# Performance work log

Measured on AMD Instinct MI355X. Metric: run time of the kernel, lower is better.

## Reference

```python
import jax, jax.numpy as jnp
import numpy as np

N = 100000      # n_nodes
E = 1600000     # n_edges (avg degree 16)
IN_C = 256
OUT_C = 64
HID = OUT_C * 2  # 128


def setup_inputs() -> dict:
    key = jax.random.key(0)
    k = jax.random.split(key, 4)
    x = jax.random.normal(k[0], (N, IN_C), dtype=jnp.float32)
    edge_index = jax.random.randint(k[1], (2, E), 0, N, dtype=jnp.int64)
    W1 = jax.random.normal(k[2], (IN_C, HID), dtype=jnp.float32) * (1.0 / np.sqrt(IN_C))
    b1 = jnp.zeros((HID,), dtype=jnp.float32)
    W2 = jax.random.normal(k[3], (HID, OUT_C), dtype=jnp.float32) * (1.0 / np.sqrt(HID))
    b2 = jnp.zeros((OUT_C,), dtype=jnp.float32)
    return {"x": x, "edge_index": edge_index, "W1": W1, "b1": b1, "W2": W2, "b2": b2}


def reference(x, edge_index, W1, b1, W2, b2):
    n = x.shape[0]
    # GCNConv default: add self-loops, symmetric normalization D^-1/2 A D^-1/2
    loop = jnp.arange(n, dtype=edge_index.dtype)
    src = jnp.concatenate([edge_index[0], loop])  # [E+N]
    dst = jnp.concatenate([edge_index[1], loop])  # [E+N]
    deg = jax.ops.segment_sum(jnp.ones_like(dst, dtype=x.dtype), dst, num_segments=n)
    dis = jax.lax.rsqrt(deg)  # deg >= 1 thanks to self-loops
    norm = dis[src] * dis[dst]  # [E+N]

    def gcn_conv(h, W, b):
        h = h @ W                                   # [n, d_out] dense transform first
        msg = h[src] * norm[:, None]                # [E+N, d_out] gather + scale
        return jax.ops.segment_sum(msg, dst, num_segments=n) + b

    h = jax.nn.relu(gcn_conv(x, W1, b1))
    return gcn_conv(h, W2, b2)
```

## Files before the change

kernel.cpp:

```cpp
#include <hip/hip_runtime.h>
#include <hip/hip_bf16.h>


#define GCN_IN_C 256
#define GCN_HID  128
#define GCN_OUT  64

#define BKT_SHIFT 8
#define BKT_NODES 256
#define EPB 4096

typedef __bf16 bf16x8 __attribute__((ext_vector_type(8)));
typedef __bf16 bf16x4 __attribute__((ext_vector_type(4)));
typedef float f32x4 __attribute__((ext_vector_type(4)));

__global__ __launch_bounds__(256) void k_bucket_hist(const int* __restrict__ dst,
                                                     int* __restrict__ bcnt, int e, int nb) {
  __shared__ int h[512];
  int tid = threadIdx.x;
  h[tid] = 0; h[tid + 256] = 0;
  __syncthreads();
  int base = blockIdx.x * EPB;
#pragma unroll
  for (int j = 0; j < EPB / 256; ++j) {
    int i = base + j * 256 + tid;
    if (i < e) atomicAdd(&h[dst[i] >> BKT_SHIFT], 1);
  }
  __syncthreads();
  if (tid < nb && h[tid]) atomicAdd(&bcnt[tid], h[tid]);
  if (tid + 256 < nb && h[tid + 256]) atomicAdd(&bcnt[tid + 256], h[tid + 256]);
}

__global__ __launch_bounds__(512) void k_scan_buckets(const int* __restrict__ bcnt,
                                                      int* __restrict__ bbase,
                                                      int* __restrict__ bcur, int nb) {
  __shared__ int sh[512];
  int t = threadIdx.x;
  int v = (t < nb) ? bcnt[t] : 0;
  sh[t] = v;
  __syncthreads();
  for (int d = 1; d < 512; d <<= 1) {
    int x = (t >= d) ? sh[t - d] : 0;
    __syncthreads();
    sh[t] += x;
    __syncthreads();
  }
  if (t < nb) {
    int ex = sh[t] - v;
    bbase[t] = ex;
    bcur[t] = ex;
  }
}

__global__ __launch_bounds__(256) void k_partition(const int* __restrict__ src,
                                                   const int* __restrict__ dst,
                                                   int* __restrict__ bcur,
                                                   unsigned int* __restrict__ part,
                                                   int e, int nb) {
  __shared__ int h[512];
  __shared__ int base[512];
  int tid = threadIdx.x;
  h[tid] = 0; h[tid + 256] = 0;
  __syncthreads();
  int b0 = blockIdx.x * EPB;
  int s[EPB / 256], d[EPB / 256], rk[EPB / 256];
#pragma unroll
  for (int j = 0; j < EPB / 256; ++j) {
    int i = b0 + j * 256 + tid;
    if (i < e) {
      s[j] = src[i];
      d[j] = dst[i];
      rk[j] = atomicAdd(&h[d[j] >> BKT_SHIFT], 1);
    }
  }
  __syncthreads();
  if (tid < nb && h[tid]) base[tid] = atomicAdd(&bcur[tid], h[tid]);
  if (tid + 256 < nb && h[tid + 256]) base[tid + 256] = atomicAdd(&bcur[tid + 256], h[tid + 256]);
  __syncthreads();
#pragma unroll
  for (int j = 0; j < EPB / 256; ++j) {
    int i = b0 + j * 256 + tid;
    if (i < e) {
      int bk = d[j] >> BKT_SHIFT;
      unsigned int dl = (unsigned int)(d[j] & (BKT_NODES - 1));
      part[base[bk] + rk[j]] = (dl << 24) | (unsigned int)s[j];
    }
  }
}

__global__ __launch_bounds__(256) void k_bucket_csr(
    const unsigned int* __restrict__ part, const int* __restrict__ bbase,
    const int* __restrict__ bcnt, int* __restrict__ off, int* __restrict__ end,
    float* __restrict__ dis, int* __restrict__ csr, int n) {
  __shared__ int cnt[256];
  __shared__ int sc[256];
  __shared__ int cur[256];
  int b = blockIdx.x, tid = threadIdx.x;
  int node0 = b << BKT_SHIFT;
  int eb0 = bbase[b];
  int ebn = bcnt[b];
  cnt[tid] = 0;
  __syncthreads();
  for (int i = tid; i < ebn; i += 256) atomicAdd(&cnt[part[eb0 + i] >> 24], 1);
  __syncthreads();
  int v = cnt[tid];
  sc[tid] = v;
  __syncthreads();
  for (int dd = 1; dd < 256; dd <<= 1) {
    int x = (tid >= dd) ? sc[tid - dd] : 0;
    __syncthreads();
    sc[tid] += x;
    __syncthreads();
  }
  int lo = sc[tid] - v;
  cur[tid] = lo;
  int node = node0 + tid;
  if (node < n) {
    off[node] = eb0 + lo;
    end[node] = eb0 + lo + v;
    dis[node] = rsqrtf((float)v + 1.0f);
  }
  __syncthreads();
  for (int i = tid; i < ebn; i += 256) {
    unsigned int u = part[eb0 + i];
    int r = atomicAdd(&cur[u >> 24], 1);
    csr[eb0 + r] = (int)(u & 0xFFFFFFu);
  }
}

template<int K, int NOUT>
__device__ __forceinline__ void split_w_one(const float* __restrict__ W,
                                            __bf16* __restrict__ Wsp, int idx) {
  int n = idx % NOUT;
  int g = (idx / NOUT) & 3;
  int ks = idx / (4 * NOUT);
  __bf16* hi = Wsp + (size_t)ks * (2 * 4 * NOUT * 8) + ((size_t)g * NOUT + n) * 8;
  __bf16* lo = hi + 4 * NOUT * 8;
#pragma unroll
  for (int j = 0; j < 8; ++j) {
    float f = W[(size_t)(ks * 32 + g * 8 + j) * NOUT + n];
    __bf16 h = (__bf16)f;
    hi[j] = h;
    lo[j] = (__bf16)(f - (float)h);
  }
}

__global__ __launch_bounds__(256) void k_split_w_all(
    const float* __restrict__ W1, __bf16* __restrict__ w1sp,
    const float* __restrict__ W2, __bf16* __restrict__ w2sp) {
  constexpr int N1 = (GCN_IN_C / 32) * 4 * GCN_HID;
  constexpr int N2 = (GCN_HID / 32) * 4 * GCN_OUT;
  int idx = blockIdx.x * 256 + threadIdx.x;
  if (idx < N1) split_w_one<GCN_IN_C, GCN_HID>(W1, w1sp, idx);
  else if (idx < N1 + N2) split_w_one<GCN_HID, GCN_OUT>(W2, w2sp, idx - N1);
}

template<int K, int NOUT>
__global__ __launch_bounds__(256) void k_gemm_l1(
    const float* __restrict__ X, const __bf16* __restrict__ Wsp,
    const float* __restrict__ dis, __bf16* __restrict__ T, int M) {
  constexpr int KSTEPS = K / 32;
  constexpr int NF = NOUT / 16;
  constexpr int TILE = 2 * 4 * NOUT * 8;
  constexpr int HI = 4 * NOUT * 8;
  __shared__ __bf16 lds[KSTEPS * HI];

  const int tid = threadIdx.x;
  const int wave = tid >> 6;
  const int lane = tid & 63;
  const int l15 = lane & 15;
  const int lg = lane >> 4;
  const int r0w = blockIdx.x * 64 + wave * 16;

  {
    constexpr int CHUNKS = KSTEPS * HI * 2 / 1024;
#pragma unroll
    for (int it = 0; it < CHUNKS / 4; ++it) {
      int c = it * 4 + wave;
      int ks = c >> 3;
      int ci = c & 7;
      const char* gs = (const char*)(Wsp + (size_t)ks * TILE) + ci * 1024 + lane * 16;
      char* ls = (char*)lds + (size_t)ks * HI * 2 + ci * 1024;
      __builtin_amdgcn_global_load_lds(
          (const __attribute__((address_space(1))) void*)gs,
          (__attribute__((address_space(3))) void*)ls, 16, 0, 0);
    }
  }

  f32x4 acc[NF];
#pragma unroll
  for (int nf = 0; nf < NF; ++nf) acc[nf] = (f32x4){0.f, 0.f, 0.f, 0.f};

  int row = r0w + l15;
  int rowA = (row < M) ? row : (M - 1);

  const int boff = lg * NOUT * 8 + l15 * 8;

  auto loadA = [&](int ks, float4* v0, float4* v1) {
    const float* ap = X + (size_t)rowA * K + ks * 32 + lg * 8;
    *v0 = *(const float4*)ap;
    *v1 = *(const float4*)(ap + 4);
  };
  auto loadBL = [&](int ks, bf16x8* bl) {
    const __bf16* wl = Wsp + (size_t)ks * TILE + HI + boff;
#pragma unroll
    for (int nf = 0; nf < NF; ++nf) bl[nf] = *(const bf16x8*)(wl + nf * 128);
  };

  float4 ca0, ca1, na0, na1;
  bf16x8 blc[NF], bln[NF];
  loadA(0, &ca0, &ca1);
  loadBL(0, blc);
  __syncthreads();

#pragma unroll 1
  for (int ks = 0; ks < KSTEPS; ++ks) {
    if (ks + 1 < KSTEPS) {
      loadA(ks + 1, &na0, &na1);
      loadBL(ks + 1, bln);
    }
    bf16x8 ah, al;
    {
      float va[8] = {ca0.x, ca0.y, ca0.z, ca0.w, ca1.x, ca1.y, ca1.z, ca1.w};
#pragma unroll
      for (int j = 0; j < 8; ++j) {
        __bf16 h = (__bf16)va[j];
        ah[j] = h;
        al[j] = (__bf16)(va[j] - (float)h);
      }
    }
    const __bf16* lh = lds + (size_t)ks * HI + boff;
#pragma unroll
    for (int nf = 0; nf < NF; ++nf) {
      bf16x8 bh = *(const bf16x8*)(lh + nf * 128);
      acc[nf] = __builtin_amdgcn_mfma_f32_16x16x32_bf16(bh, ah, acc[nf], 0, 0, 0);
      acc[nf] = __builtin_amdgcn_mfma_f32_16x16x32_bf16(blc[nf], ah, acc[nf], 0, 0, 0);
      acc[nf] = __builtin_amdgcn_mfma_f32_16x16x32_bf16(bh, al, acc[nf], 0, 0, 0);
    }
    ca0 = na0; ca1 = na1;
#pragma unroll
    for (int nf = 0; nf < NF; ++nf) blc[nf] = bln[nf];
  }

  if (row < M) {
    float dv = dis[row];
#pragma unroll
    for (int nf = 0; nf < NF; ++nf) {
      bf16x4 pk;
#pragma unroll
      for (int r = 0; r < 4; ++r) pk[r] = (__bf16)(dv * acc[nf][r]);
      *(bf16x4*)(T + (size_t)row * NOUT + nf * 16 + lg * 4) = pk;
    }
  }
}

template<int K, int NOUT>
__global__ __launch_bounds__(256) void k_gemm_l2(
    const __bf16* __restrict__ A, const __bf16* __restrict__ Wsp,
    const float* __restrict__ dis, __bf16* __restrict__ T, int M) {
  constexpr int KSTEPS = K / 32;
  constexpr int NF = NOUT / 16;
  constexpr int TILE = 2 * 4 * NOUT * 8;
  constexpr int HL = 4 * NOUT * 8;
  __shared__ __bf16 lds[KSTEPS * TILE];

  const int tid = threadIdx.x;
  const int wave = tid >> 6;
  const int lane = tid & 63;
  const int l15 = lane & 15;
  const int lg = lane >> 4;
  const int r0w = blockIdx.x * 64 + wave * 16;

  {
    constexpr int CHUNKS = KSTEPS * TILE * 2 / 1024;
#pragma unroll
    for (int it = 0; it < CHUNKS / 4; ++it) {
      int c = it * 4 + wave;
      const char* gs = (const char*)Wsp + c * 1024 + lane * 16;
      char* ls = (char*)lds + c * 1024;
      __builtin_amdgcn_global_load_lds(
          (const __attribute__((address_space(1))) void*)gs,
          (__attribute__((address_space(3))) void*)ls, 16, 0, 0);
    }
  }

  f32x4 acc[NF];
#pragma unroll
  for (int nf = 0; nf < NF; ++nf) acc[nf] = (f32x4){0.f, 0.f, 0.f, 0.f};

  int row = r0w + l15;
  int rowA = (row < M) ? row : (M - 1);
  const int boff = lg * NOUT * 8 + l15 * 8;

  bf16x8 ca, na;
  ca = *(const bf16x8*)(A + (size_t)rowA * K + lg * 8);
  __syncthreads();

#pragma unroll 1
  for (int ks = 0; ks < KSTEPS; ++ks) {
    if (ks + 1 < KSTEPS)
      na = *(const bf16x8*)(A + (size_t)rowA * K + (ks + 1) * 32 + lg * 8);
    const __bf16* lh = lds + (size_t)ks * TILE + boff;
    const __bf16* ll = lh + HL;
#pragma unroll
    for (int nf = 0; nf < NF; ++nf) {
      bf16x8 bh = *(const bf16x8*)(lh + nf * 128);
      bf16x8 bl = *(const bf16x8*)(ll + nf * 128);
      acc[nf] = __builtin_amdgcn_mfma_f32_16x16x32_bf16(bh, ca, acc[nf], 0, 0, 0);
      acc[nf] = __builtin_amdgcn_mfma_f32_16x16x32_bf16(bl, ca, acc[nf], 0, 0, 0);
    }
    ca = na;
  }

  if (row < M) {
    float dv = dis[row];
#pragma unroll
    for (int nf = 0; nf < NF; ++nf) {
      bf16x4 pk;
#pragma unroll
      for (int r = 0; r < 4; ++r) pk[r] = (__bf16)(dv * acc[nf][r]);
      *(bf16x4*)(T + (size_t)row * NOUT + nf * 16 + lg * 4) = pk;
    }
  }
}

template<int C, bool RELU, typename OutT>
__global__ __launch_bounds__(256) void k_agg_csr(
    const int* __restrict__ csr, const int* __restrict__ off,
    const int* __restrict__ end, const __bf16* __restrict__ ts,
    const float* __restrict__ dis, const float* __restrict__ bias,
    OutT* __restrict__ out, int n) {
  constexpr int LPG = C / 8;
  int gtid = blockIdx.x * 256 + threadIdx.x;
  int node = gtid / LPG;
  int gl = gtid % LPG;
  if (node >= n) return;

  float acc[8];
  {
    bf16x8 v = *(const bf16x8*)(ts + (size_t)node * C + gl * 8);
#pragma unroll
    for (int j = 0; j < 8; ++j) acc[j] = (float)v[j];
  }

  int e = off[node];
  int e1 = end[node];
  for (; e + 4 <= e1; e += 4) {
    int s0 = csr[e];
    int s1 = csr[e + 1];
    int s2 = csr[e + 2];
    int s3 = csr[e + 3];
    bf16x8 v0 = *(const bf16x8*)(ts + (size_t)s0 * C + gl * 8);
    bf16x8 v1 = *(const bf16x8*)(ts + (size_t)s1 * C + gl * 8);
    bf16x8 v2 = *(const bf16x8*)(ts + (size_t)s2 * C + gl * 8);
    bf16x8 v3 = *(const bf16x8*)(ts + (size_t)s3 * C + gl * 8);
#pragma unroll
    for (int j = 0; j < 8; ++j)
      acc[j] += ((float)v0[j] + (float)v1[j]) + ((float)v2[j] + (float)v3[j]);
  }
  for (; e < e1; ++e) {
    int s0 = csr[e];
    bf16x8 v0 = *(const bf16x8*)(ts + (size_t)s0 * C + gl * 8);
#pragma unroll
    for (int j = 0; j < 8; ++j) acc[j] += (float)v0[j];
  }

  float di = dis[node];
  float o[8];
#pragma unroll
  for (int j = 0; j < 8; ++j) {
    o[j] = di * acc[j] + bias[gl * 8 + j];
    if (RELU) o[j] = fmaxf(o[j], 0.f);
  }
  if constexpr (sizeof(OutT) == 2) {
    bf16x8 pv;
#pragma unroll
    for (int j = 0; j < 8; ++j) pv[j] = (__bf16)o[j];
    *(bf16x8*)((__bf16*)out + (size_t)node * C + gl * 8) = pv;
  } else {
    float4* op = (float4*)((float*)out + (size_t)node * C + gl * 8);
    op[0] = make_float4(o[0], o[1], o[2], o[3]);
    op[1] = make_float4(o[4], o[5], o[6], o[7]);
  }
}

extern "C" void kernel_launch(void* const* d_in, const int* in_sizes, int n_in,
                              void* d_out, int out_size, void* d_ws, size_t ws_size,
                              hipStream_t stream) {
  const float* x  = (const float*)d_in[0];
  const int*   ei = (const int*)d_in[1];
  const float* W1 = (const float*)d_in[2];
  const float* b1 = (const float*)d_in[3];
  const float* W2 = (const float*)d_in[4];
  const float* b2 = (const float*)d_in[5];
  float* out = (float*)d_out;

  const int N = in_sizes[0] / GCN_IN_C;
  const int E = in_sizes[1] / 2;
  const int* src = ei;
  const int* dst = ei + E;
  const int NB = (N + BKT_NODES - 1) >> BKT_SHIFT;
  const int EB = (E + EPB - 1) / EPB;

  char* p = (char*)d_ws;
  float* dis = (float*)p;             p += (size_t)N * 4;
  __bf16* t1s = (__bf16*)p;           p += (size_t)N * GCN_HID * 2;
  __bf16* a1  = (__bf16*)p;           p += (size_t)N * GCN_HID * 2;
  int* off   = (int*)p;               p += (size_t)N * 4;
  int* end   = (int*)p;               p += (size_t)N * 4;
  int* csr   = (int*)p;               p += (size_t)E * 4;
  int* bcnt  = (int*)p;               p += 512 * 4;
  int* bbase = (int*)p;               p += 512 * 4;
  int* bcur  = (int*)p;               p += 512 * 4;
  __bf16* w1sp = (__bf16*)p;          p += (size_t)(GCN_IN_C / 32) * 2 * 4 * GCN_HID * 8 * 2;
  __bf16* w2sp = (__bf16*)p;
  unsigned int* part = (unsigned int*)a1;
  __bf16* t2s = t1s;

  k_split_w_all<<<(4096 + 1024 + 255) / 256, 256, 0, stream>>>(W1, w1sp, W2, w2sp);
  hipMemsetAsync(bcnt, 0, 512 * sizeof(int), stream);

  k_bucket_hist<<<EB, 256, 0, stream>>>(dst, bcnt, E, NB);
  k_scan_buckets<<<1, 512, 0, stream>>>(bcnt, bbase, bcur, NB);
  k_partition<<<EB, 256, 0, stream>>>(src, dst, bcur, part, E, NB);
  k_bucket_csr<<<NB, 256, 0, stream>>>(part, bbase, bcnt, off, end, dis, csr, N);

  k_gemm_l1<GCN_IN_C, GCN_HID>
      <<<(N + 63) / 64, 256, 0, stream>>>(x, w1sp, dis, t1s, N);
  k_agg_csr<GCN_HID, true, __bf16>
      <<<((size_t)N * (GCN_HID / 8) + 255) / 256, 256, 0, stream>>>(csr, off, end, t1s, dis, b1, a1, N);

  k_gemm_l2<GCN_HID, GCN_OUT>
      <<<(N + 63) / 64, 256, 0, stream>>>(a1, w2sp, dis, t2s, N);
  k_agg_csr<GCN_OUT, false, float>
      <<<((size_t)N * (GCN_OUT / 8) + 255) / 256, 256, 0, stream>>>(csr, off, end, t2s, dis, b2, out, N);
}
```

Measured before the change: 205.2 us.

## Widen layer-1 GEMM blocks, relayout low weight half, drop register prefetch

```diff
diff --git a/kernel.cpp b/kernel.cpp
--- a/kernel.cpp
+++ b/kernel.cpp
@@ -128,40 +128,50 @@
   }
 }
 
-template<int K, int NOUT>
-__device__ __forceinline__ void split_w_one(const float* __restrict__ W,
-                                            __bf16* __restrict__ Wsp, int idx) {
-  int n = idx % NOUT;
-  int g = (idx / NOUT) & 3;
-  int ks = idx / (4 * NOUT);
-  __bf16* hi = Wsp + (size_t)ks * (2 * 4 * NOUT * 8) + ((size_t)g * NOUT + n) * 8;
-  __bf16* lo = hi + 4 * NOUT * 8;
-#pragma unroll
-  for (int j = 0; j < 8; ++j) {
-    float f = W[(size_t)(ks * 32 + g * 8 + j) * NOUT + n];
-    __bf16 h = (__bf16)f;
-    hi[j] = h;
-    lo[j] = (__bf16)(f - (float)h);
-  }
-}
-
 __global__ __launch_bounds__(256) void k_split_w_all(
-    const float* __restrict__ W1, __bf16* __restrict__ w1sp,
+    const float* __restrict__ W1, __bf16* __restrict__ w1hi,
+    __bf16* __restrict__ w1lo2,
     const float* __restrict__ W2, __bf16* __restrict__ w2sp) {
   constexpr int N1 = (GCN_IN_C / 32) * 4 * GCN_HID;
   constexpr int N2 = (GCN_HID / 32) * 4 * GCN_OUT;
   int idx = blockIdx.x * 256 + threadIdx.x;
-  if (idx < N1) split_w_one<GCN_IN_C, GCN_HID>(W1, w1sp, idx);
-  else if (idx < N1 + N2) split_w_one<GCN_HID, GCN_OUT>(W2, w2sp, idx - N1);
+  if (idx < N1) {
+    int n = idx % GCN_HID;
+    int g = (idx / GCN_HID) & 3;
+    int ks = idx / (4 * GCN_HID);
+    __bf16* hi = w1hi + (size_t)ks * (4 * GCN_HID * 8) + ((size_t)g * GCN_HID + n) * 8;
+    __bf16* lo = w1lo2 + (((size_t)ks * (GCN_HID / 16) + (n >> 4)) * 64 + g * 16 + (n & 15)) * 8;
+#pragma unroll
+    for (int j = 0; j < 8; ++j) {
+      float f = W1[(size_t)(ks * 32 + g * 8 + j) * GCN_HID + n];
+      __bf16 h = (__bf16)f;
+      hi[j] = h;
+      lo[j] = (__bf16)(f - (float)h);
+    }
+  } else if (idx < N1 + N2) {
+    int i2 = idx - N1;
+    int n = i2 % GCN_OUT;
+    int g = (i2 / GCN_OUT) & 3;
+    int ks = i2 / (4 * GCN_OUT);
+    __bf16* hi = w2sp + (size_t)ks * (2 * 4 * GCN_OUT * 8) + ((size_t)g * GCN_OUT + n) * 8;
+    __bf16* lo = hi + 4 * GCN_OUT * 8;
+#pragma unroll
+    for (int j = 0; j < 8; ++j) {
+      float f = W2[(size_t)(ks * 32 + g * 8 + j) * GCN_OUT + n];
+      __bf16 h = (__bf16)f;
+      hi[j] = h;
+      lo[j] = (__bf16)(f - (float)h);
+    }
+  }
 }
 
 template<int K, int NOUT>
-__global__ __launch_bounds__(256) void k_gemm_l1(
-    const float* __restrict__ X, const __bf16* __restrict__ Wsp,
-    const float* __restrict__ dis, __bf16* __restrict__ T, int M) {
+__global__ __launch_bounds__(512, 4) void k_gemm_l1(
+    const float* __restrict__ X, const __bf16* __restrict__ Whi,
+    const __bf16* __restrict__ Wlo, const float* __restrict__ dis,
+    __bf16* __restrict__ T, int M) {
   constexpr int KSTEPS = K / 32;
   constexpr int NF = NOUT / 16;
-  constexpr int TILE = 2 * 4 * NOUT * 8;
   constexpr int HI = 4 * NOUT * 8;
   __shared__ __bf16 lds[KSTEPS * HI];
 
@@ -170,17 +180,13 @@
   const int lane = tid & 63;
   const int l15 = lane & 15;
   const int lg = lane >> 4;
-  const int r0w = blockIdx.x * 64 + wave * 16;
+  const int r0w = blockIdx.x * 128 + wave * 16;
 
   {
-    constexpr int CHUNKS = KSTEPS * HI * 2 / 1024;
-#pragma unroll
-    for (int it = 0; it < CHUNKS / 4; ++it) {
-      int c = it * 4 + wave;
-      int ks = c >> 3;
-      int ci = c & 7;
-      const char* gs = (const char*)(Wsp + (size_t)ks * TILE) + ci * 1024 + lane * 16;
-      char* ls = (char*)lds + (size_t)ks * HI * 2 + ci * 1024;
+#pragma unroll
+    for (int i = 0; i < KSTEPS * HI * 2 / (512 * 16); ++i) {
+      const char* gs = (const char*)Whi + ((size_t)i * 512 + tid) * 16;
+      char* ls = (char*)lds + (size_t)i * 8192 + wave * 1024 + lane * 16;
       __builtin_amdgcn_global_load_lds(
           (const __attribute__((address_space(1))) void*)gs,
           (__attribute__((address_space(3))) void*)ls, 16, 0, 0);
@@ -193,35 +199,22 @@
 
   int row = r0w + l15;
   int rowA = (row < M) ? row : (M - 1);
-
   const int boff = lg * NOUT * 8 + l15 * 8;
 
-  auto loadA = [&](int ks, float4* v0, float4* v1) {
-    const float* ap = X + (size_t)rowA * K + ks * 32 + lg * 8;
-    *v0 = *(const float4*)ap;
-    *v1 = *(const float4*)(ap + 4);
-  };
-  auto loadBL = [&](int ks, bf16x8* bl) {
-    const __bf16* wl = Wsp + (size_t)ks * TILE + HI + boff;
-#pragma unroll
-    for (int nf = 0; nf < NF; ++nf) bl[nf] = *(const bf16x8*)(wl + nf * 128);
-  };
-
-  float4 ca0, ca1, na0, na1;
-  bf16x8 blc[NF], bln[NF];
-  loadA(0, &ca0, &ca1);
-  loadBL(0, blc);
   __syncthreads();
 
 #pragma unroll 1
   for (int ks = 0; ks < KSTEPS; ++ks) {
-    if (ks + 1 < KSTEPS) {
-      loadA(ks + 1, &na0, &na1);
-      loadBL(ks + 1, bln);
-    }
+    const float* ap = X + (size_t)rowA * K + ks * 32 + lg * 8;
+    float4 a0 = *(const float4*)ap;
+    float4 a1 = *(const float4*)(ap + 4);
+    bf16x8 bl[NF];
+#pragma unroll
+    for (int nf = 0; nf < NF; ++nf)
+      bl[nf] = *(const bf16x8*)(Wlo + (((size_t)ks * NF + nf) * 64 + lane) * 8);
     bf16x8 ah, al;
     {
-      float va[8] = {ca0.x, ca0.y, ca0.z, ca0.w, ca1.x, ca1.y, ca1.z, ca1.w};
+      float va[8] = {a0.x, a0.y, a0.z, a0.w, a1.x, a1.y, a1.z, a1.w};
 #pragma unroll
       for (int j = 0; j < 8; ++j) {
         __bf16 h = (__bf16)va[j];
@@ -234,12 +227,9 @@
     for (int nf = 0; nf < NF; ++nf) {
       bf16x8 bh = *(const bf16x8*)(lh + nf * 128);
       acc[nf] = __builtin_amdgcn_mfma_f32_16x16x32_bf16(bh, ah, acc[nf], 0, 0, 0);
-      acc[nf] = __builtin_amdgcn_mfma_f32_16x16x32_bf16(blc[nf], ah, acc[nf], 0, 0, 0);
+      acc[nf] = __builtin_amdgcn_mfma_f32_16x16x32_bf16(bl[nf], ah, acc[nf], 0, 0, 0);
       acc[nf] = __builtin_amdgcn_mfma_f32_16x16x32_bf16(bh, al, acc[nf], 0, 0, 0);
     }
-    ca0 = na0; ca1 = na1;
-#pragma unroll
-    for (int nf = 0; nf < NF; ++nf) blc[nf] = bln[nf];
   }
 
   if (row < M) {
@@ -412,12 +402,13 @@
   int* bcnt  = (int*)p;               p += 512 * 4;
   int* bbase = (int*)p;               p += 512 * 4;
   int* bcur  = (int*)p;               p += 512 * 4;
-  __bf16* w1sp = (__bf16*)p;          p += (size_t)(GCN_IN_C / 32) * 2 * 4 * GCN_HID * 8 * 2;
-  __bf16* w2sp = (__bf16*)p;
+  __bf16* w1hi  = (__bf16*)p;         p += (size_t)(GCN_IN_C / 32) * 4 * GCN_HID * 8 * 2;
+  __bf16* w1lo2 = (__bf16*)p;         p += (size_t)(GCN_IN_C / 32) * 4 * GCN_HID * 8 * 2;
+  __bf16* w2sp  = (__bf16*)p;
   unsigned int* part = (unsigned int*)a1;
   __bf16* t2s = t1s;
 
-  k_split_w_all<<<(4096 + 1024 + 255) / 256, 256, 0, stream>>>(W1, w1sp, W2, w2sp);
+  k_split_w_all<<<(4096 + 1024 + 255) / 256, 256, 0, stream>>>(W1, w1hi, w1lo2, W2, w2sp);
   hipMemsetAsync(bcnt, 0, 512 * sizeof(int), stream);
 
   k_bucket_hist<<<EB, 256, 0, stream>>>(dst, bcnt, E, NB);
@@ -426,7 +417,7 @@
   k_bucket_csr<<<NB, 256, 0, stream>>>(part, bbase, bcnt, off, end, dis, csr, N);
 
   k_gemm_l1<GCN_IN_C, GCN_HID>
-      <<<(N + 63) / 64, 256, 0, stream>>>(x, w1sp, dis, t1s, N);
+      <<<(N + 127) / 128, 512, 0, stream>>>(x, w1hi, w1lo2, dis, t1s, N);
   k_agg_csr<GCN_HID, true, __bf16>
       <<<((size_t)N * (GCN_HID / 8) + 255) / 256, 256, 0, stream>>>(csr, off, end, t1s, dis, b1, a1, N);
 
```

After: 207.5 us. No clear change (+1.2%).
